# Kernel tuning notes

Hardware: AMD Instinct MI355X
Metric: run time of the kernel (lower is better)

Reference implementation:

```python
import jax, jax.numpy as jnp
import numpy as np
import math

D_MODEL = 1024
D_HEAD = 64
N_HEADS = D_MODEL // D_HEAD  # 16
COND = 768
EPS = 1e-6


def make_freqs():
    # AxialRoPE(dim=d_head//2, n_heads): freqs linspace in log-space, reshaped [dim//4, nh].T
    dim = D_HEAD // 2  # 32
    n = N_HEADS * dim // 4  # 128
    log_min = math.log(math.pi)
    log_max = math.log(10.0 * math.pi)
    freqs = jnp.exp(jnp.linspace(log_min, log_max, n + 1, dtype=jnp.float32)[:-1])
    return freqs.reshape(dim // 4, N_HEADS).T  # [n_heads, d_head//8] = [16, 8]


def setup_inputs() -> dict:
    key = jax.random.key(0)
    ks = jax.random.split(key, 6)
    N, H, W = 8, 32, 32
    x = jax.random.normal(ks[0], (N, H, W, D_MODEL), jnp.float32)
    pos = jax.random.uniform(ks[1], (N, H, W, 2), jnp.float32) * 2.0 - 1.0
    cond = jax.random.normal(ks[2], (N, COND), jnp.float32)
    norm_w = jax.random.normal(ks[3], (D_MODEL, COND), jnp.float32) * 0.02
    qkv_w = jax.random.normal(ks[4], (3 * D_MODEL, D_MODEL), jnp.float32) / math.sqrt(D_MODEL)
    out_w = jax.random.normal(ks[5], (D_MODEL, D_MODEL), jnp.float32) * 0.02
    scale = jnp.full((N_HEADS,), 10.0, jnp.float32)
    return {"x": x, "pos": pos, "cond": cond, "norm_w": norm_w,
            "qkv_w": qkv_w, "out_w": out_w, "scale": scale}


def rms_norm(x, scale, eps):
    mean_sq = jnp.mean(x * x, axis=-1, keepdims=True)
    return x * (scale * jax.lax.rsqrt(mean_sq + eps))


def apply_rotary(x, theta):
    # rotate first 2*d dims of the head; rest passes through
    d = theta.shape[-1]
    x1, x2, rest = x[..., :d], x[..., d:2 * d], x[..., 2 * d:]
    cos, sin = jnp.cos(theta), jnp.sin(theta)
    return jnp.concatenate([x1 * cos - x2 * sin, x2 * cos + x1 * sin, rest], axis=-1)


def reference(x, pos, cond, norm_w, qkv_w, out_w, scale):
    N, H, W, _ = x.shape
    S = H * W
    skip = x
    # AdaRMSNorm: scale = zero-init linear(cond) + 1
    ns = cond @ norm_w.T  # [N, d_model]
    xn = rms_norm(x, ns[:, None, None, :] + 1.0, EPS)
    # QKV projection, split 'n h w (t nh e)'
    qkv = (xn @ qkv_w.T).reshape(N, S, 3, N_HEADS, D_HEAD)
    q = jnp.transpose(qkv[:, :, 0], (0, 2, 1, 3))  # [N, nh, S, e]
    k = jnp.transpose(qkv[:, :, 1], (0, 2, 1, 3))
    v = jnp.transpose(qkv[:, :, 2], (0, 2, 1, 3))
    # cosine-sim scaling: per-head learned scale, L2-normalize q,k
    sqrt_scale = jnp.sqrt(scale)[:, None, None]  # [nh,1,1]
    q = q * (sqrt_scale * jax.lax.rsqrt(jnp.sum(q * q, -1, keepdims=True) + EPS))
    k = k * (sqrt_scale * jax.lax.rsqrt(jnp.sum(k * k, -1, keepdims=True) + EPS))
    # axial RoPE theta
    freqs = make_freqs()  # [nh, d_head//8]
    pos_f = pos.reshape(N, S, 2)
    theta_h = pos_f[:, :, None, 0:1] * freqs  # [N,S,nh,8]
    theta_w = pos_f[:, :, None, 1:2] * freqs
    theta = jnp.concatenate([theta_h, theta_w], axis=-1)  # [N,S,nh,16]
    theta = jnp.transpose(theta, (0, 2, 1, 3))  # [N,nh,S,16]
    q = apply_rotary(q, theta)
    k = apply_rotary(k, theta)
    # attention with scale=1.0 (cosine-sim already scaled)
    scores = jnp.einsum('bhqe,bhke->bhqk', q, k)
    probs = jax.nn.softmax(scores, axis=-1)
    o = jnp.einsum('bhqk,bhke->bhqe', probs, v)  # [N,nh,S,e]
    o = jnp.transpose(o, (0, 2, 1, 3)).reshape(N, H, W, D_MODEL)
    return o @ out_w.T + skip
```

## Files before the change

### kernel.cpp

```cpp
#include <hip/hip_runtime.h>
#include <hip/hip_bf16.h>
#include <math.h>

typedef __bf16 bf16;
typedef __bf16 bf16x8 __attribute__((ext_vector_type(8)));
typedef __bf16 bf16x4 __attribute__((ext_vector_type(4)));
typedef float f32x4 __attribute__((ext_vector_type(4)));

#define MFMA16(a, b, c) __builtin_amdgcn_mfma_f32_16x16x32_bf16((a), (b), (c), 0, 0, 0)

__device__ __forceinline__ void gload_lds16(const void* g, void* l) {
  __builtin_amdgcn_global_load_lds((__attribute__((address_space(1))) void*)(g),
                                   (__attribute__((address_space(3))) void*)(l),
                                   16, 0, 0);
}

__global__ __launch_bounds__(256) void f2bf_kernel(const float* __restrict__ in,
                                                   bf16* __restrict__ out, int n4) {
  int i = blockIdx.x * 256 + threadIdx.x;
  if (i >= n4) return;
  float4 v = ((const float4*)in)[i];
  bf16x4 o;
  o[0] = (bf16)v.x; o[1] = (bf16)v.y; o[2] = (bf16)v.z; o[3] = (bf16)v.w;
  *(bf16x4*)(out + (size_t)i * 4) = o;
}

__global__ __launch_bounds__(256) void ns_kernel(const float* __restrict__ cond,
                                                 const float* __restrict__ norm_w,
                                                 float* __restrict__ nsp1) {
  int tid = blockIdx.x * 256 + threadIdx.x;
  int b = tid >> 10, c = tid & 1023;
  const float4* wv = (const float4*)(norm_w + (size_t)c * 768);
  const float4* cv = (const float4*)(cond + (size_t)b * 768);
  float acc = 0.f;
#pragma unroll 8
  for (int i = 0; i < 192; ++i) {
    float4 w4 = wv[i], c4 = cv[i];
    acc += w4.x * c4.x + w4.y * c4.y + w4.z * c4.z + w4.w * c4.w;
  }
  nsp1[tid] = acc + 1.0f;
}

__global__ __launch_bounds__(256) void rmsnorm_kernel(const float* __restrict__ x,
                                                      const float* __restrict__ nsp1,
                                                      bf16* __restrict__ xn) {
  int lane = threadIdx.x & 63, w = threadIdx.x >> 6;
  int m = blockIdx.x * 4 + w;
  int b = m >> 10;
  const float* xp = x + (size_t)m * 1024 + lane * 16;
  float v[16];
  float ss = 0.f;
#pragma unroll
  for (int i = 0; i < 4; ++i) {
    float4 t4 = ((const float4*)xp)[i];
    v[4 * i + 0] = t4.x; v[4 * i + 1] = t4.y; v[4 * i + 2] = t4.z; v[4 * i + 3] = t4.w;
    ss += t4.x * t4.x + t4.y * t4.y + t4.z * t4.z + t4.w * t4.w;
  }
#pragma unroll
  for (int off = 32; off >= 1; off >>= 1) ss += __shfl_xor(ss, off);
  float r = rsqrtf(ss * (1.0f / 1024.0f) + 1e-6f);
  const float* np = nsp1 + (size_t)b * 1024 + lane * 16;
  bf16x8 o0, o1;
#pragma unroll
  for (int j = 0; j < 8; ++j) o0[j] = (bf16)(v[j] * np[j] * r);
#pragma unroll
  for (int j = 0; j < 8; ++j) o1[j] = (bf16)(v[8 + j] * np[8 + j] * r);
  bf16* op = xn + (size_t)m * 1024 + lane * 16;
  *(bf16x8*)op = o0;
  *(bf16x8*)(op + 8) = o1;
}

template <int MODE>
__global__ __launch_bounds__(512, 2) void gemm256b(const bf16* __restrict__ A,
                                                   const bf16* __restrict__ B, int nbn,
                                                   bf16* __restrict__ qout, bf16* __restrict__ kout,
                                                   bf16* __restrict__ vtout, float* __restrict__ fout,
                                                   const float* __restrict__ skip) {
  constexpr int K = 1024;
  __shared__ __align__(16) bf16 sm[24576];
  const int t = threadIdx.x;
  const int cpx = gridDim.x >> 3;
  const int bid = blockIdx.x;
  const int virt = (bid & 7) * cpx + (bid >> 3);
  const int bn = virt % nbn, bm = virt / nbn;
  const int m0 = bm * 256, n0 = bn * 128;
  const int lane = t & 63, wid = t >> 6;
  const int wr = wid >> 1, wc = wid & 1;
  const int r16 = lane & 15, hi = lane >> 4;

  const int tq = t >> 3, c8 = t & 7, cp = c8 ^ (tq & 7);
  const size_t gA = (size_t)(m0 + tq * 2 + (cp >> 2)) * K + (cp & 3) * 8;
  const size_t gB = (size_t)(n0 + tq * 2 + (cp >> 2)) * K + (cp & 3) * 8;
  const size_t gj = (size_t)128 * K;
  const int ldst = t * 8;

  const int chunk = ((r16 & 1) * 4 + hi) ^ (r16 >> 1);
  int aoff[4], boff[4];
#pragma unroll
  for (int fr = 0; fr < 4; ++fr) aoff[fr] = (wr * 32 + fr * 8 + (r16 >> 1)) * 64 + chunk * 8;
#pragma unroll
  for (int fc = 0; fc < 4; ++fc)
    boff[fc] = (wc * 32 + fc * 8 + (r16 >> 1)) * 64 + chunk * 8 + 8192;

  f32x4 acc[4][4] = {};
  constexpr int NS = K >> 5;

#define STG(tile, slot)                                              \
  {                                                                  \
    const bf16* as_ = A + gA + (size_t)(tile) * 32;                  \
    const bf16* bs_ = B + gB + (size_t)(tile) * 32;                  \
    gload_lds16(as_, &sm[(slot) * 12288 + ldst]);                    \
    gload_lds16(as_ + gj, &sm[(slot) * 12288 + 4096 + ldst]);        \
    gload_lds16(bs_, &sm[(slot) * 12288 + 8192 + ldst]);             \
  }

  STG(0, 0);
  STG(1, 1);

  for (int s = 0; s < NS; ++s) {
    if (s < NS - 1) {
      asm volatile("s_waitcnt vmcnt(3)" ::: "memory");
    } else {
      asm volatile("s_waitcnt vmcnt(0)" ::: "memory");
    }
    __builtin_amdgcn_s_barrier();
    __builtin_amdgcn_sched_barrier(0);
    bf16x8 af[4], bfr[4];
    const bf16* base = &sm[(s & 1) * 12288];
#pragma unroll
    for (int fr = 0; fr < 4; ++fr) af[fr] = *(const bf16x8*)&base[aoff[fr]];
#pragma unroll
    for (int fc = 0; fc < 4; ++fc) bfr[fc] = *(const bf16x8*)&base[boff[fc]];
    asm volatile("s_waitcnt lgkmcnt(0)" ::: "memory");
    __builtin_amdgcn_sched_barrier(0);
    __builtin_amdgcn_s_barrier();
    __builtin_amdgcn_sched_barrier(0);
    if (s + 2 < NS) STG(s + 2, s & 1);
    __builtin_amdgcn_s_setprio(1);
#pragma unroll
    for (int fc = 0; fc < 4; ++fc)
#pragma unroll
      for (int fr = 0; fr < 4; ++fr) acc[fr][fc] = MFMA16(af[fr], bfr[fc], acc[fr][fc]);
    __builtin_amdgcn_s_setprio(0);
  }
#undef STG

  if constexpr (MODE == 0) {
    const int p = n0 >> 10;
#pragma unroll
    for (int fr = 0; fr < 4; ++fr) {
      int mrow = m0 + wr * 64 + fr * 16 + hi * 4;
      int b = mrow >> 10, s0 = mrow & 1023;
#pragma unroll
      for (int fc = 0; fc < 4; ++fc) {
        int n = n0 + wc * 64 + fc * 16 + r16;
        int d = n & 63, hh = (n >> 6) & 15;
        if (p == 2) {
          bf16x4 pk;
          pk[0] = (bf16)acc[fr][fc][0]; pk[1] = (bf16)acc[fr][fc][1];
          pk[2] = (bf16)acc[fr][fc][2]; pk[3] = (bf16)acc[fr][fc][3];
          *(bf16x4*)&vtout[(((size_t)(b * 16 + hh) * 64 + d) << 10) + s0] = pk;
        } else {
          bf16* dst = (p == 0) ? qout : kout;
#pragma unroll
          for (int r = 0; r < 4; ++r)
            dst[(((size_t)(b * 16 + hh) << 10) + s0 + r) * 64 + d] = (bf16)acc[fr][fc][r];
        }
      }
    }
  } else {
#pragma unroll
    for (int fr = 0; fr < 4; ++fr) {
      int mrow = m0 + wr * 64 + fr * 16 + hi * 4;
#pragma unroll
      for (int fc = 0; fc < 4; ++fc) {
        int n = n0 + wc * 64 + fc * 16 + r16;
#pragma unroll
        for (int r = 0; r < 4; ++r) {
          size_t off = (size_t)(mrow + r) * 1024 + n;
          fout[off] = acc[fr][fc][r] + skip[off];
        }
      }
    }
  }
}

__device__ __forceinline__ void qk_process(bf16* p, float sq, const float* cth, const float* sth) {
  float vv[64];
  float ss = 0.f;
#pragma unroll
  for (int i = 0; i < 8; ++i) {
    bf16x8 tv = *(const bf16x8*)(p + i * 8);
#pragma unroll
    for (int e = 0; e < 8; ++e) {
      float f = (float)tv[e];
      vv[i * 8 + e] = f;
      ss += f * f;
    }
  }
  float r = sq * rsqrtf(ss + 1e-6f);
#pragma unroll
  for (int i = 0; i < 64; ++i) vv[i] *= r;
#pragma unroll
  for (int i = 0; i < 16; ++i) {
    float x1 = vv[i], x2 = vv[i + 16];
    vv[i] = x1 * cth[i] - x2 * sth[i];
    vv[i + 16] = x2 * cth[i] + x1 * sth[i];
  }
#pragma unroll
  for (int i = 0; i < 8; ++i) {
    bf16x8 o;
#pragma unroll
    for (int e = 0; e < 8; ++e) o[e] = (bf16)vv[i * 8 + e];
    *(bf16x8*)(p + i * 8) = o;
  }
}

__global__ __launch_bounds__(256) void prep_kernel(bf16* __restrict__ q, bf16* __restrict__ k,
                                                   const float* __restrict__ pos,
                                                   const float* __restrict__ scale) {
  int tid = blockIdx.x * 256 + threadIdx.x;
  int b = tid >> 14, h = (tid >> 10) & 15, s = tid & 1023;
  float ph = pos[((size_t)b * 1024 + s) * 2 + 0];
  float pw = pos[((size_t)b * 1024 + s) * 2 + 1];
  float cth[16], sth[16];
  const float logpi = 1.14472988584940017f;
  const float stp = 0.0179897502011134460f;
#pragma unroll
  for (int j = 0; j < 8; ++j) {
    float f = __expf(logpi + stp * (float)(j * 16 + h));
    float th = ph * f, tw = pw * f;
    cth[j] = __cosf(th); sth[j] = __sinf(th);
    cth[8 + j] = __cosf(tw); sth[8 + j] = __sinf(tw);
  }
  float sq = sqrtf(scale[h]);
  const float LOG2E = 1.4426950408889634f;
  qk_process(q + (size_t)tid * 64, sq * LOG2E, cth, sth);
  qk_process(k + (size_t)tid * 64, sq, cth, sth);
}

__global__ __launch_bounds__(256) void attn_kernel(const bf16* __restrict__ q,
                                                   const bf16* __restrict__ k,
                                                   const bf16* __restrict__ vt,
                                                   bf16* __restrict__ o) {
  int bid = blockIdx.x;
  int virt = (bid & 7) * 256 + (bid >> 3);
  const int bh = virt >> 4;
  const int qt = virt & 15;
  const int b = bh >> 4, h = bh & 15;
  const int t = threadIdx.x, lane = t & 63, w = t >> 6;
  const int r16 = lane & 15, hi = lane >> 4;
  const int swp = r16 & 7;

  __shared__ bf16 lK[2][4096];
  __shared__ bf16 lV[2][4096];
  __shared__ bf16 lP[4][1024];
  bf16* myp = lP[w];

  const bf16* kp = k + (size_t)bh * 65536;
  const bf16* vp = vt + (size_t)bh * 65536;

  const bf16* qp = q + ((size_t)bh * 1024 + qt * 64 + w * 16) * 64;
  bf16x8 aq0 = *(const bf16x8*)&qp[r16 * 64 + hi * 8];
  bf16x8 aq1 = *(const bf16x8*)&qp[r16 * 64 + 32 + hi * 8];

  bf16x8 ones;
#pragma unroll
  for (int i = 0; i < 8; ++i) ones[i] = (bf16)1.0f;

  const int srow0 = t >> 3, sc0 = t & 7;

  f32x4 oacc[4] = {};
  f32x4 lacc = {};

#pragma unroll
  for (int j = 0; j < 2; ++j) {
    int row = srow0 + j * 32;
    int se = ((sc0 ^ (row & 7)) << 3);
    gload_lds16(kp + (size_t)row * 64 + se, &lK[0][t * 8 + j * 2048]);
    gload_lds16(vp + (size_t)row * 1024 + se, &lV[0][t * 8 + j * 2048]);
  }
  __syncthreads();

  int cur = 0;
  for (int kt = 0; kt < 16; ++kt) {
    if (kt < 15) {
      const bf16* kt_base = kp + (kt + 1) * 4096;
      const bf16* vt_base = vp + (kt + 1) * 64;
#pragma unroll
      for (int j = 0; j < 2; ++j) {
        int row = srow0 + j * 32;
        int se = ((sc0 ^ (row & 7)) << 3);
        gload_lds16(kt_base + (size_t)row * 64 + se, &lK[cur ^ 1][t * 8 + j * 2048]);
        gload_lds16(vt_base + (size_t)row * 1024 + se, &lV[cur ^ 1][t * 8 + j * 2048]);
      }
    }
    f32x4 sT[4] = {};
    __builtin_amdgcn_s_setprio(1);
#pragma unroll
    for (int c = 0; c < 4; ++c) {
      int row = c * 16 + r16, sw = row & 7;
      bf16x8 bk0 = *(const bf16x8*)&lK[cur][row * 64 + ((hi ^ sw) << 3)];
      bf16x8 bk1 = *(const bf16x8*)&lK[cur][row * 64 + (((hi + 4) ^ sw) << 3)];
      sT[c] = MFMA16(bk0, aq0, sT[c]);
      sT[c] = MFMA16(bk1, aq1, sT[c]);
    }
    __builtin_amdgcn_s_setprio(0);
    bf16x4 pb[4];
#pragma unroll
    for (int c = 0; c < 4; ++c) {
#pragma unroll
      for (int r = 0; r < 4; ++r) pb[c][r] = (bf16)exp2f(sT[c][r]);
    }
#pragma unroll
    for (int c = 0; c < 4; ++c) {
      int eoff = r16 * 64 + (((c * 32 + hi * 8) ^ (swp << 4)) >> 1);
      *(bf16x4*)&myp[eoff] = pb[c];
    }
    {
      bf16x8 pa0 = *(const bf16x8*)&myp[r16 * 64 + ((hi ^ swp) << 3)];
      bf16x8 pa1 = *(const bf16x8*)&myp[r16 * 64 + (((hi + 4) ^ swp) << 3)];
      __builtin_amdgcn_s_setprio(1);
#pragma unroll
      for (int c = 0; c < 4; ++c) {
        int row = c * 16 + r16, sw = row & 7;
        bf16x8 bv0 = *(const bf16x8*)&lV[cur][row * 64 + ((hi ^ sw) << 3)];
        bf16x8 bv1 = *(const bf16x8*)&lV[cur][row * 64 + (((hi + 4) ^ sw) << 3)];
        oacc[c] = MFMA16(pa0, bv0, oacc[c]);
        oacc[c] = MFMA16(pa1, bv1, oacc[c]);
      }
      lacc = MFMA16(pa0, ones, lacc);
      lacc = MFMA16(pa1, ones, lacc);
      __builtin_amdgcn_s_setprio(0);
    }
    __syncthreads();
    cur ^= 1;
  }
  f32x4 inv;
#pragma unroll
  for (int r = 0; r < 4; ++r) inv[r] = 1.f / lacc[r];
#pragma unroll
  for (int c = 0; c < 4; ++c) {
#pragma unroll
    for (int r = 0; r < 4; ++r) {
      int srow = qt * 64 + w * 16 + hi * 4 + r;
      o[((size_t)b * 1024 + srow) * 1024 + h * 64 + c * 16 + r16] =
          (bf16)(oacc[c][r] * inv[r]);
    }
  }
}

extern "C" void kernel_launch(void* const* d_in, const int* in_sizes, int n_in,
                              void* d_out, int out_size, void* d_ws, size_t ws_size,
                              hipStream_t stream) {
  const float* x      = (const float*)d_in[0];
  const float* pos    = (const float*)d_in[1];
  const float* cond   = (const float*)d_in[2];
  const float* norm_w = (const float*)d_in[3];
  const float* qkv_w  = (const float*)d_in[4];
  const float* out_w  = (const float*)d_in[5];
  const float* scale  = (const float*)d_in[6];
  float* out = (float*)d_out;

  char* ws = (char*)d_ws;
  bf16* xn        = (bf16*)(ws + 0);
  bf16* qkv_w_bf  = (bf16*)(ws + 16777216);
  bf16* out_w_bf  = (bf16*)(ws + 23068672);
  float* nsp1     = (float*)(ws + 25165824);
  bf16* qraw      = (bf16*)(ws + 25198592);
  bf16* kraw      = (bf16*)(ws + 41975808);
  bf16* vt        = (bf16*)(ws + 58753024);
  bf16* o_attn    = xn;

  f2bf_kernel<<<3072, 256, 0, stream>>>(qkv_w, qkv_w_bf, 786432);
  f2bf_kernel<<<1024, 256, 0, stream>>>(out_w, out_w_bf, 262144);
  ns_kernel<<<32, 256, 0, stream>>>(cond, norm_w, nsp1);
  rmsnorm_kernel<<<2048, 256, 0, stream>>>(x, nsp1, xn);
  gemm256b<0><<<768, 512, 0, stream>>>(xn, qkv_w_bf, 24, qraw, kraw, vt, nullptr, nullptr);
  prep_kernel<<<512, 256, 0, stream>>>(qraw, kraw, pos, scale);
  attn_kernel<<<2048, 256, 0, stream>>>(qraw, kraw, vt, o_attn);
  gemm256b<1><<<256, 512, 0, stream>>>(o_attn, out_w_bf, 8, nullptr, nullptr, nullptr, out, x);
}
```

Baseline: 219.4 us.

## Fuse Q/K cosine-normalization and axial RoPE into QKV GEMM epilogue

Moves the per-head L2 normalization, learned scale and axial rotary embedding of q and k into the QKV GEMM epilogue. Each wave's 64-column tile is exactly one head, so the sum of squares is reduced with lane shuffles across the 16 columns. This removes the separate prep kernel, which re-read and re-wrote q and k in global memory. The attention kernel also gets a min-blocks-per-CU launch bound of 4, which limits its registers. The trade-off is a heavier GEMM epilogue with per-element sincos and pos loads, plus scalar bf16 stores.

Measured after the change: 198.8 us. -9.4%, faster.

```diff
diff --git a/kernel.cpp b/kernel.cpp
--- a/kernel.cpp
+++ b/kernel.cpp
@@ -75,7 +75,9 @@
                                                    const bf16* __restrict__ B, int nbn,
                                                    bf16* __restrict__ qout, bf16* __restrict__ kout,
                                                    bf16* __restrict__ vtout, float* __restrict__ fout,
-                                                   const float* __restrict__ skip) {
+                                                   const float* __restrict__ skip,
+                                                   const float* __restrict__ pos,
+                                                   const float* __restrict__ scale) {
   constexpr int K = 1024;
   __shared__ __align__(16) bf16 sm[24576];
   const int t = threadIdx.x;
@@ -147,24 +149,57 @@
 
   if constexpr (MODE == 0) {
     const int p = n0 >> 10;
-#pragma unroll
-    for (int fr = 0; fr < 4; ++fr) {
-      int mrow = m0 + wr * 64 + fr * 16 + hi * 4;
-      int b = mrow >> 10, s0 = mrow & 1023;
-#pragma unroll
-      for (int fc = 0; fc < 4; ++fc) {
-        int n = n0 + wc * 64 + fc * 16 + r16;
-        int d = n & 63, hh = (n >> 6) & 15;
-        if (p == 2) {
+    if (p == 2) {
+#pragma unroll
+      for (int fr = 0; fr < 4; ++fr) {
+        int mrow = m0 + wr * 64 + fr * 16 + hi * 4;
+        int b = mrow >> 10, s0 = mrow & 1023;
+#pragma unroll
+        for (int fc = 0; fc < 4; ++fc) {
+          int n = n0 + wc * 64 + fc * 16 + r16;
+          int d = n & 63, hh = (n >> 6) & 15;
           bf16x4 pk;
           pk[0] = (bf16)acc[fr][fc][0]; pk[1] = (bf16)acc[fr][fc][1];
           pk[2] = (bf16)acc[fr][fc][2]; pk[3] = (bf16)acc[fr][fc][3];
           *(bf16x4*)&vtout[(((size_t)(b * 16 + hh) * 64 + d) << 10) + s0] = pk;
-        } else {
-          bf16* dst = (p == 0) ? qout : kout;
-#pragma unroll
-          for (int r = 0; r < 4; ++r)
-            dst[(((size_t)(b * 16 + hh) << 10) + s0 + r) * 64 + d] = (bf16)acc[fr][fc][r];
+        }
+      }
+    } else {
+      const int hh = ((n0 + wc * 64) >> 6) & 15;
+      const float LOG2E = 1.4426950408889634f;
+      const float sqv = sqrtf(scale[hh]) * (p == 0 ? LOG2E : 1.0f);
+      const float f = __expf(1.14472988584940017f +
+                             0.0179897502011134460f * (float)((r16 & 7) * 16 + hh));
+      const bool is_h = (r16 < 8);
+      bf16* dst = (p == 0) ? qout : kout;
+#pragma unroll
+      for (int fr = 0; fr < 4; ++fr) {
+        int mrow = m0 + wr * 64 + fr * 16 + hi * 4;
+        int b = mrow >> 10, s0 = mrow & 1023;
+        float rr[4];
+#pragma unroll
+        for (int r = 0; r < 4; ++r) {
+          float ss = acc[fr][0][r] * acc[fr][0][r] + acc[fr][1][r] * acc[fr][1][r] +
+                     acc[fr][2][r] * acc[fr][2][r] + acc[fr][3][r] * acc[fr][3][r];
+          ss += __shfl_xor(ss, 1);
+          ss += __shfl_xor(ss, 2);
+          ss += __shfl_xor(ss, 4);
+          ss += __shfl_xor(ss, 8);
+          rr[r] = sqv * rsqrtf(ss + 1e-6f);
+        }
+#pragma unroll
+        for (int r = 0; r < 4; ++r) {
+          float2 pp = *(const float2*)&pos[(((size_t)b << 10) + s0 + r) * 2];
+          float th = (is_h ? pp.x : pp.y) * f;
+          float sv, cv;
+          __sincosf(th, &sv, &cv);
+          float x1 = acc[fr][0][r] * rr[r];
+          float x2 = acc[fr][1][r] * rr[r];
+          size_t rowb = (((size_t)(b * 16 + hh) << 10) + s0 + r) * 64;
+          dst[rowb + r16]      = (bf16)(x1 * cv - x2 * sv);
+          dst[rowb + 16 + r16] = (bf16)(x2 * cv + x1 * sv);
+          dst[rowb + 32 + r16] = (bf16)(acc[fr][2][r] * rr[r]);
+          dst[rowb + 48 + r16] = (bf16)(acc[fr][3][r] * rr[r]);
         }
       }
     }
@@ -185,64 +220,10 @@
   }
 }
 
-__device__ __forceinline__ void qk_process(bf16* p, float sq, const float* cth, const float* sth) {
-  float vv[64];
-  float ss = 0.f;
-#pragma unroll
-  for (int i = 0; i < 8; ++i) {
-    bf16x8 tv = *(const bf16x8*)(p + i * 8);
-#pragma unroll
-    for (int e = 0; e < 8; ++e) {
-      float f = (float)tv[e];
-      vv[i * 8 + e] = f;
-      ss += f * f;
-    }
-  }
-  float r = sq * rsqrtf(ss + 1e-6f);
-#pragma unroll
-  for (int i = 0; i < 64; ++i) vv[i] *= r;
-#pragma unroll
-  for (int i = 0; i < 16; ++i) {
-    float x1 = vv[i], x2 = vv[i + 16];
-    vv[i] = x1 * cth[i] - x2 * sth[i];
-    vv[i + 16] = x2 * cth[i] + x1 * sth[i];
-  }
-#pragma unroll
-  for (int i = 0; i < 8; ++i) {
-    bf16x8 o;
-#pragma unroll
-    for (int e = 0; e < 8; ++e) o[e] = (bf16)vv[i * 8 + e];
-    *(bf16x8*)(p + i * 8) = o;
-  }
-}
-
-__global__ __launch_bounds__(256) void prep_kernel(bf16* __restrict__ q, bf16* __restrict__ k,
-                                                   const float* __restrict__ pos,
-                                                   const float* __restrict__ scale) {
-  int tid = blockIdx.x * 256 + threadIdx.x;
-  int b = tid >> 14, h = (tid >> 10) & 15, s = tid & 1023;
-  float ph = pos[((size_t)b * 1024 + s) * 2 + 0];
-  float pw = pos[((size_t)b * 1024 + s) * 2 + 1];
-  float cth[16], sth[16];
-  const float logpi = 1.14472988584940017f;
-  const float stp = 0.0179897502011134460f;
-#pragma unroll
-  for (int j = 0; j < 8; ++j) {
-    float f = __expf(logpi + stp * (float)(j * 16 + h));
-    float th = ph * f, tw = pw * f;
-    cth[j] = __cosf(th); sth[j] = __sinf(th);
-    cth[8 + j] = __cosf(tw); sth[8 + j] = __sinf(tw);
-  }
-  float sq = sqrtf(scale[h]);
-  const float LOG2E = 1.4426950408889634f;
-  qk_process(q + (size_t)tid * 64, sq * LOG2E, cth, sth);
-  qk_process(k + (size_t)tid * 64, sq, cth, sth);
-}
-
-__global__ __launch_bounds__(256) void attn_kernel(const bf16* __restrict__ q,
-                                                   const bf16* __restrict__ k,
-                                                   const bf16* __restrict__ vt,
-                                                   bf16* __restrict__ o) {
+__global__ __launch_bounds__(256, 4) void attn_kernel(const bf16* __restrict__ q,
+                                                      const bf16* __restrict__ k,
+                                                      const bf16* __restrict__ vt,
+                                                      bf16* __restrict__ o) {
   int bid = blockIdx.x;
   int virt = (bid & 7) * 256 + (bid >> 3);
   const int bh = virt >> 4;
@@ -376,8 +357,9 @@
   f2bf_kernel<<<1024, 256, 0, stream>>>(out_w, out_w_bf, 262144);
   ns_kernel<<<32, 256, 0, stream>>>(cond, norm_w, nsp1);
   rmsnorm_kernel<<<2048, 256, 0, stream>>>(x, nsp1, xn);
-  gemm256b<0><<<768, 512, 0, stream>>>(xn, qkv_w_bf, 24, qraw, kraw, vt, nullptr, nullptr);
-  prep_kernel<<<512, 256, 0, stream>>>(qraw, kraw, pos, scale);
+  gemm256b<0><<<768, 512, 0, stream>>>(xn, qkv_w_bf, 24, qraw, kraw, vt, nullptr, nullptr,
+                                       pos, scale);
   attn_kernel<<<2048, 256, 0, stream>>>(qraw, kraw, vt, o_attn);
-  gemm256b<1><<<256, 512, 0, stream>>>(o_attn, out_w_bf, 8, nullptr, nullptr, nullptr, out, x);
-}
+  gemm256b<1><<<256, 512, 0, stream>>>(o_attn, out_w_bf, 8, nullptr, nullptr, nullptr, out, x,
+                                       nullptr, nullptr);
+}
```
